# Optimization experiments

Measured on AMD Instinct MI355X. Metric: run time of the kernel, lower is better.

Reference implementation:

```python
import jax, jax.numpy as jnp
import numpy as np

H = 48  # hidden_size


def _lstm_cell(inp, h, c, Wih, Whh, bih, bhh):
    # PyTorch LSTMCell: gates ordered (i, f, g, o)
    gates = inp @ Wih.T + h @ Whh.T + bih + bhh
    i, f, g, o = jnp.split(gates, 4, axis=-1)
    i = jax.nn.sigmoid(i)
    f = jax.nn.sigmoid(f)
    g = jnp.tanh(g)
    o = jax.nn.sigmoid(o)
    c_new = f * c + i * g
    h_new = o * jnp.tanh(c_new)
    return h_new, c_new


def setup_inputs() -> dict:
    key = jax.random.key(0)
    ks = jax.random.split(key, 8)
    B, T = 4096, 512
    s = 0.1
    return {
        "x": jax.random.normal(ks[0], (B, T), dtype=jnp.float32),
        "W_ih0": jax.random.normal(ks[1], (4 * H, 1), dtype=jnp.float32) * s,
        "W_hh0": jax.random.normal(ks[2], (4 * H, H), dtype=jnp.float32) * s,
        "b_ih0": jnp.full((4 * H,), 0.01, dtype=jnp.float32),
        "b_hh0": jnp.full((4 * H,), 0.01, dtype=jnp.float32),
        "W_ih1": jax.random.normal(ks[3], (4 * H, H), dtype=jnp.float32) * s,
        "W_hh1": jax.random.normal(ks[4], (4 * H, H), dtype=jnp.float32) * s,
        "b_ih1": jnp.full((4 * H,), 0.01, dtype=jnp.float32),
        "b_hh1": jnp.full((4 * H,), 0.01, dtype=jnp.float32),
        "W_lin": jax.random.normal(ks[5], (1, H), dtype=jnp.float32) * s,
        "b_lin": jnp.full((1,), 0.01, dtype=jnp.float32),
        "future_pred": 64,
    }


def reference(x, W_ih0, W_hh0, b_ih0, b_hh0, W_ih1, W_hh1, b_ih1, b_hh1,
              W_lin, b_lin, future_pred):
    B = x.shape[0]
    h0 = jnp.zeros((B, H), dtype=jnp.float32)
    c0 = jnp.zeros((B, H), dtype=jnp.float32)
    h1 = jnp.zeros((B, H), dtype=jnp.float32)
    c1 = jnp.zeros((B, H), dtype=jnp.float32)

    def tick(h0, c0, h1, c1, inp):  # inp: [B,1]
        h0, c0 = _lstm_cell(inp, h0, c0, W_ih0, W_hh0, b_ih0, b_hh0)
        h1, c1 = _lstm_cell(h0, h1, c1, W_ih1, W_hh1, b_ih1, b_hh1)
        out = h1 @ W_lin.T + b_lin  # [B,1]
        return h0, c0, h1, c1, out

    # teacher-forced pass over observed sequence
    def step_obs(carry, xt):
        h0, c0, h1, c1 = carry
        h0, c0, h1, c1, out = tick(h0, c0, h1, c1, xt)
        return (h0, c0, h1, c1), out

    xs = jnp.swapaxes(x, 0, 1)[:, :, None]  # [T, B, 1]
    (h0, c0, h1, c1), outs_obs = jax.lax.scan(step_obs, (h0, c0, h1, c1), xs)
    last_out = outs_obs[-1]

    def step_fut(carry, _):
        h0, c0, h1, c1, out = carry
        h0, c0, h1, c1, out = tick(h0, c0, h1, c1, out)
        return (h0, c0, h1, c1, out), out

    _, outs_fut = jax.lax.scan(step_fut, (h0, c0, h1, c1, last_out), None,
                               length=future_pred)

    outs = jnp.concatenate([outs_obs, outs_fut], axis=0)  # [T+F, B, 1]
    return jnp.swapaxes(outs[:, :, 0], 0, 1)  # [B, T+F]
```

## Files before the change

kernel.cpp:

```cpp
#include <hip/hip_runtime.h>

#define T_OBS 512
#define RSTRH 264
#define PSTR  28
#define L2E   1.44269504089f

typedef float    f32x4 __attribute__((ext_vector_type(4)));
typedef _Float16 f16x8 __attribute__((ext_vector_type(8)));

#define MF(A,B,C) __builtin_amdgcn_mfma_f32_16x16x32_f16(A,B,C,0,0,0)

__device__ __forceinline__ unsigned f2h(float f){
    union { _Float16 h; unsigned short u; } v; v.h=(_Float16)f; return (unsigned)v.u;
}

__device__ __forceinline__ float act1(const f32x4 a, float& c){
    const float Ei=__builtin_amdgcn_exp2f(a[0]), Ef=__builtin_amdgcn_exp2f(a[1]);
    const float Eg=__builtin_amdgcn_exp2f(a[2]), Eo=__builtin_amdgcn_exp2f(a[3]);
    const float ui=1.f+Ei, uf=1.f+Ef, ug=1.f+Eg, uo=1.f+Eo;
    const float P=ui*uf, Q=ug*uo;
    const float R=__builtin_amdgcn_rcpf(P*Q);
    const float aP=R*Q, aQ=R*P;
    const float ig=aP*uf, fg=aP*ui;
    const float og=aQ*ug;
    const float gg=fmaf(aQ*uo,-2.f,1.f);
    c = fg*c + ig*gg;
    const float Ec=__builtin_amdgcn_exp2f(2.f*L2E*c);
    return og*fmaf(__builtin_amdgcn_rcpf(1.f+Ec),-2.f,1.f);
}

__device__ __forceinline__ int u_of_pos(const int p){
    return 8*(p>>3) + 4*(p&1) + ((p&7)>>1);
}

__global__ __launch_bounds__(768, 1) void lstm2_v8(
    const float* __restrict__ x,
    const float* __restrict__ Wih0, const float* __restrict__ Whh0,
    const float* __restrict__ bih0, const float* __restrict__ bhh0,
    const float* __restrict__ Wih1, const float* __restrict__ Whh1,
    const float* __restrict__ bih1, const float* __restrict__ bhh1,
    const float* __restrict__ Wlin, const float* __restrict__ blin,
    const int* __restrict__ fut,
    float* __restrict__ out)
{
    __shared__ __attribute__((aligned(16))) _Float16 s_h[16 * RSTRH];
    __shared__ __attribute__((aligned(16))) float s_pr[2][16 * PSTR];
    unsigned* const s32 = (unsigned*)s_h;

    const int tid  = threadIdx.x;
    const int wave = tid >> 6, lane = tid & 63;
    const int q    = lane & 15, rg = lane >> 4;
    const bool isL1 = (wave >= 6);
    const int  w    = isL1 ? wave - 6 : wave;

    for (int i = tid; i < 16 * RSTRH; i += 768) s_h[i] = (_Float16)0.f;

    const float sgl = ((q & 3) == 2) ? 2.f * L2E : -L2E;

    f16x8 ah[2][3], al[2][3];
    #pragma unroll
    for (int i = 0; i < 2; ++i) {
        const int t  = 2 * w + i;
        const int rp = 16 * t + q;
        const int r0 = (rp & 3) * 48 + (rp >> 2);
        #pragma unroll
        for (int s = 0; s < 3; ++s)
            #pragma unroll
            for (int j = 0; j < 8; ++j) {
                const int p = 32 * s + 8 * rg + j;
                float v = 0.f;
                if (isL1) v = ((p < 48) ? Wih1[r0 * 48 + u_of_pos(p)]
                                        : Whh1[r0 * 48 + u_of_pos(p - 48)]) * sgl;
                else if (p < 48) v = Whh0[r0 * 48 + u_of_pos(p)] * sgl;
                const _Float16 hi = (_Float16)v;
                ah[i][s][j] = hi;
                al[i][s][j] = (_Float16)(v - (float)hi);
            }
    }

    const float sg4[4] = { -L2E, -L2E, 2.f * L2E, -L2E };
    f32x4 bvt[2], wi0v[2];
    float wlq[2];
    #pragma unroll
    for (int i = 0; i < 2; ++i) {
        const int u = 8 * w + 4 * i + rg;
        wlq[i] = Wlin[u];
        #pragma unroll
        for (int g = 0; g < 4; ++g) {
            bvt[i][g]  = (isL1 ? (bih1[g*48+u] + bhh1[g*48+u])
                               : (bih0[g*48+u] + bhh0[g*48+u])) * sg4[g];
            wi0v[i][g] = Wih0[g * 48 + u] * sg4[g];
        }
    }

    int koff[3];
    #pragma unroll
    for (int s = 0; s < 3; ++s) {
        const int p0 = 32 * s + 8 * rg;
        koff[s] = p0 + ((p0 >= 48) ? 80 : 0);
    }

    const int F    = fut[0];
    const int TT   = T_OBS + F;
    const int bb0  = blockIdx.x * 16;
    const float bl = blin[0];
    const int xrow = (bb0 + q) * T_OBS;
    const int nbh  = q * RSTRH;
    const int hwp  = nbh + (isL1 ? 128 : 0) + 8 * w + 2 * rg;
    const int prw  = q * PSTR + 4 * w + rg;

    float cc0 = 0.f, cc1 = 0.f;
    const f32x4 z4 = { 0.f, 0.f, 0.f, 0.f };

    __syncthreads();

    if (!isL1) {
        const float x0 = x[xrow];
        const f32x4 a0 = bvt[0] + wi0v[0] * x0;
        const f32x4 a1 = bvt[1] + wi0v[1] * x0;
        const unsigned h0 = f2h(act1(a0, cc0));
        const unsigned h1 = f2h(act1(a1, cc1));
        s32[hwp >> 1] = h0 | (h1 << 16);
    }
    __syncthreads();
    float xcur = isL1 ? 0.f : x[xrow + 1];

#define STEADY(TAU_, CB_, PB_) do {                                              \
    if (!isL1) {                                                                 \
        const float xnxt = x[xrow + (((TAU_) + 1 < T_OBS) ? (TAU_) + 1 : T_OBS - 1)]; \
        if ((TAU_) >= 2 && wave == 0) {           \
            const int nn = lane >> 2, j0 = lane & 3;                             \
            const float* pr = &s_pr[((TAU_) - 1) & 1][nn * PSTR];                \
            float sg = pr[j0] + pr[j0+4] + pr[j0+8] + pr[j0+12]                  \
                     + pr[j0+16] + pr[j0+20];                                    \
            sg += __shfl_xor(sg, 1); sg += __shfl_xor(sg, 2);                    \
            if (j0 == 0) out[(bb0 + nn) * TT + ((TAU_) - 2)] = sg + bl;          \
        }                                                                        \
        const f16x8 B0 = *(const f16x8*)(s_h + nbh + (PB_) + koff[0]);           \
        const f16x8 B1 = *(const f16x8*)(s_h + nbh + (PB_) + koff[1]);           \
        f32x4 Aq[2], Bq[2];                                                      \
        _Pragma("unroll")                                                        \
        for (int i = 0; i < 2; ++i) {                                            \
            Aq[i] = MF(ah[i][0], B0, bvt[i]);                                    \
            Aq[i] = MF(al[i][0], B0, Aq[i]);                                     \
            Bq[i] = MF(ah[i][1], B1, z4);                                        \
            Bq[i] = MF(al[i][1], B1, Bq[i]);                                     \
        }                                                                        \
        const f32x4 a0 = Aq[0] + Bq[0] + wi0v[0] * xcur;                         \
        const f32x4 a1 = Aq[1] + Bq[1] + wi0v[1] * xcur;                         \
        const unsigned h0 = f2h(act1(a0, cc0));                                  \
        const unsigned h1 = f2h(act1(a1, cc1));                                  \
        s32[(hwp + (CB_)) >> 1] = h0 | (h1 << 16);                               \
        xcur = xnxt;                                                             \
    } else {                                                                     \
        const f16x8 B0 = *(const f16x8*)(s_h + nbh + (PB_) + koff[0]);           \
        const f16x8 B1 = *(const f16x8*)(s_h + nbh + (PB_) + koff[1]);           \
        const f16x8 B2 = *(const f16x8*)(s_h + nbh + (PB_) + koff[2]);           \
        f32x4 Aq[2], Bq[2];                                                      \
        _Pragma("unroll")                                                        \
        for (int i = 0; i < 2; ++i) {                                            \
            Aq[i] = MF(ah[i][0], B0, bvt[i]);                                    \
            Aq[i] = MF(al[i][0], B0, Aq[i]);                                     \
            Aq[i] = MF(ah[i][1], B1, Aq[i]);                                     \
            Bq[i] = MF(al[i][1], B1, z4);                                        \
            Bq[i] = MF(ah[i][2], B2, Bq[i]);                                     \
            Bq[i] = MF(al[i][2], B2, Bq[i]);                                     \
        }                                                                        \
        const f32x4 a0 = Aq[0] + Bq[0];                                          \
        const f32x4 a1 = Aq[1] + Bq[1];                                          \
        const float h0 = act1(a0, cc0);                                          \
        const float h1 = act1(a1, cc1);                                          \
        s32[(hwp + (CB_)) >> 1] = f2h(h0) | (f2h(h1) << 16);                     \
        s_pr[(TAU_) & 1][prw] = fmaf(h1, wlq[1], h0 * wlq[0]);                   \
    }                                                                            \
    __syncthreads();                                                             \
} while (0)

    for (int tau = 1; tau < T_OBS - 1; tau += 2) {
        STEADY(tau,     64, 0);
        STEADY(tau + 1,  0, 64);
    }
    STEADY(T_OBS - 1, 64, 0);

    if (tid < 16) {
        const float* pr = &s_pr[1][tid * PSTR];
        const f32x4 sv = *(const f32x4*)(pr)      + *(const f32x4*)(pr + 4)
                       + *(const f32x4*)(pr + 8)  + *(const f32x4*)(pr + 12)
                       + *(const f32x4*)(pr + 16) + *(const f32x4*)(pr + 20);
        out[(bb0 + tid) * TT + (T_OBS - 2)] = sv[0] + sv[1] + sv[2] + sv[3] + bl;
    }

    for (int tau = T_OBS; tau <= TT; ++tau) {
        const int cb = (tau & 1) * 64;
        const int pb = cb ^ 64;

        f32x4 Aq[2], Bq[2];
        if (isL1) {
            const f16x8 B0 = *(const f16x8*)(s_h + nbh + pb + koff[0]);
            const f16x8 B1 = *(const f16x8*)(s_h + nbh + pb + koff[1]);
            const f16x8 B2 = *(const f16x8*)(s_h + nbh + pb + koff[2]);
            #pragma unroll
            for (int i = 0; i < 2; ++i) {
                Aq[i] = MF(ah[i][0], B0, bvt[i]);
                Aq[i] = MF(al[i][0], B0, Aq[i]);
                Aq[i] = MF(ah[i][1], B1, Aq[i]);
                Bq[i] = MF(al[i][1], B1, z4);
                Bq[i] = MF(ah[i][2], B2, Bq[i]);
                Bq[i] = MF(al[i][2], B2, Bq[i]);
            }
            const f32x4 a0 = Aq[0] + Bq[0];
            const f32x4 a1 = Aq[1] + Bq[1];
            const float h0 = act1(a0, cc0);
            const float h1 = act1(a1, cc1);
            s32[(hwp + cb) >> 1] = f2h(h0) | (f2h(h1) << 16);
            s_pr[tau & 1][prw] = fmaf(h1, wlq[1], h0 * wlq[0]);
        } else {
            const f16x8 B0 = *(const f16x8*)(s_h + nbh + pb + koff[0]);
            const f16x8 B1 = *(const f16x8*)(s_h + nbh + pb + koff[1]);
            #pragma unroll
            for (int i = 0; i < 2; ++i) {
                Aq[i] = MF(ah[i][0], B0, bvt[i]);
                Aq[i] = MF(al[i][0], B0, Aq[i]);
                Bq[i] = MF(ah[i][1], B1, z4);
                Bq[i] = MF(al[i][1], B1, Bq[i]);
            }
        }
        __syncthreads();

        if (!isL1) {
            const float* pr = &s_pr[tau & 1][q * PSTR];
            const f32x4 sv = *(const f32x4*)(pr)      + *(const f32x4*)(pr + 4)
                           + *(const f32x4*)(pr + 8)  + *(const f32x4*)(pr + 12)
                           + *(const f32x4*)(pr + 16) + *(const f32x4*)(pr + 20);
            const float o = sv[0] + sv[1] + sv[2] + sv[3] + bl;
            if (tid < 16) out[(bb0 + q) * TT + (tau - 1)] = o;
            if (tau < TT) {
                const f32x4 a0 = Aq[0] + Bq[0] + wi0v[0] * o;
                const f32x4 a1 = Aq[1] + Bq[1] + wi0v[1] * o;
                const unsigned h0 = f2h(act1(a0, cc0));
                const unsigned h1 = f2h(act1(a1, cc1));
                s32[(hwp + cb) >> 1] = h0 | (h1 << 16);
            }
        }
        __syncthreads();
    }
}

extern "C" void kernel_launch(void* const* d_in, const int* in_sizes, int n_in,
                              void* d_out, int out_size, void* d_ws, size_t ws_size,
                              hipStream_t stream) {
    const float* x    = (const float*)d_in[0];
    const float* Wih0 = (const float*)d_in[1];
    const float* Whh0 = (const float*)d_in[2];
    const float* bih0 = (const float*)d_in[3];
    const float* bhh0 = (const float*)d_in[4];
    const float* Wih1 = (const float*)d_in[5];
    const float* Whh1 = (const float*)d_in[6];
    const float* bih1 = (const float*)d_in[7];
    const float* bhh1 = (const float*)d_in[8];
    const float* Wlin = (const float*)d_in[9];
    const float* blin = (const float*)d_in[10];
    const int*   fut  = (const int*)d_in[11];
    float* out = (float*)d_out;

    const int B    = in_sizes[0] / T_OBS;
    const int grid = B / 16;
    lstm2_v8<<<grid, 768, 0, stream>>>(
        x, Wih0, Whh0, bih0, bhh0, Wih1, Whh1, bih1, bhh1, Wlin, blin, fut, out);
}
```

Before: 512.9 us.

## Replace block barriers with LDS counter spin-waits and triple-buffered hidden state

```diff
diff --git a/kernel.cpp b/kernel.cpp
--- a/kernel.cpp
+++ b/kernel.cpp
@@ -1,7 +1,7 @@
 #include <hip/hip_runtime.h>
 
 #define T_OBS 512
-#define RSTRH 264
+#define RSTRH 296
 #define PSTR  28
 #define L2E   1.44269504089f
 
@@ -33,7 +33,16 @@
     return 8*(p>>3) + 4*(p&1) + ((p&7)>>1);
 }
 
-__global__ __launch_bounds__(768, 1) void lstm2_v8(
+__device__ __forceinline__ void spin_ge(volatile unsigned* pc, unsigned t0, unsigned t1){
+    unsigned v = *pc;
+    while (((v & 0xffffu) < t0) || ((v >> 16) < t1)) {
+        __builtin_amdgcn_s_sleep(1);
+        v = *pc;
+    }
+    asm volatile("" ::: "memory");
+}
+
+__global__ __launch_bounds__(768, 1) void lstm2_v9(
     const float* __restrict__ x,
     const float* __restrict__ Wih0, const float* __restrict__ Whh0,
     const float* __restrict__ bih0, const float* __restrict__ bhh0,
@@ -44,8 +53,10 @@
     float* __restrict__ out)
 {
     __shared__ __attribute__((aligned(16))) _Float16 s_h[16 * RSTRH];
-    __shared__ __attribute__((aligned(16))) float s_pr[2][16 * PSTR];
+    __shared__ __attribute__((aligned(16))) float s_pr[3][16 * PSTR];
+    __shared__ unsigned s_cnt;
     unsigned* const s32 = (unsigned*)s_h;
+    volatile unsigned* const pcv = (volatile unsigned*)&s_cnt;
 
     const int tid  = threadIdx.x;
     const int wave = tid >> 6, lane = tid & 63;
@@ -54,6 +65,7 @@
     const int  w    = isL1 ? wave - 6 : wave;
 
     for (int i = tid; i < 16 * RSTRH; i += 768) s_h[i] = (_Float16)0.f;
+    if (tid == 0) s_cnt = 0u;
 
     const float sgl = ((q & 3) == 2) ? 2.f * L2E : -L2E;
 
@@ -93,24 +105,17 @@
         }
     }
 
-    int koff[3];
-    #pragma unroll
-    for (int s = 0; s < 3; ++s) {
-        const int p0 = 32 * s + 8 * rg;
-        koff[s] = p0 + ((p0 >= 48) ? 80 : 0);
-    }
-
+    const int ko0 = 8 * rg, ko1 = 32 + 8 * rg, ko2 = 64 + 8 * rg;
     const int F    = fut[0];
     const int TT   = T_OBS + F;
     const int bb0  = blockIdx.x * 16;
     const float bl = blin[0];
     const int xrow = (bb0 + q) * T_OBS;
     const int nbh  = q * RSTRH;
-    const int hwp  = nbh + (isL1 ? 128 : 0) + 8 * w + 2 * rg;
+    const int hw0  = nbh + 8 * w + 2 * rg;
     const int prw  = q * PSTR + 4 * w + rg;
 
     float cc0 = 0.f, cc1 = 0.f;
-    const f32x4 z4 = { 0.f, 0.f, 0.f, 0.f };
 
     __syncthreads();
 
@@ -118,131 +123,146 @@
         const float x0 = x[xrow];
         const f32x4 a0 = bvt[0] + wi0v[0] * x0;
         const f32x4 a1 = bvt[1] + wi0v[1] * x0;
-        const unsigned h0 = f2h(act1(a0, cc0));
-        const unsigned h1 = f2h(act1(a1, cc1));
-        s32[hwp >> 1] = h0 | (h1 << 16);
-    }
-    __syncthreads();
+        const unsigned h0p = f2h(act1(a0, cc0));
+        const unsigned h1p = f2h(act1(a1, cc1));
+        s32[hw0 >> 1] = h0p | (h1p << 16);
+        asm volatile("s_waitcnt lgkmcnt(0)" ::: "memory");
+        if (lane == 0) atomicAdd(&s_cnt, 1u);
+    } else {
+        if (lane == 0) atomicAdd(&s_cnt, 1u << 16);
+    }
     float xcur = isL1 ? 0.f : x[xrow + 1];
 
-#define STEADY(TAU_, CB_, PB_) do {                                              \
+#define STEADY(TAU_, WR_, RR_, GB_) do {                                         \
+    const unsigned t0_ = 6u * (unsigned)(TAU_);                                  \
     if (!isL1) {                                                                 \
+        spin_ge(pcv, t0_, t0_ - 6u);                                             \
         const float xnxt = x[xrow + (((TAU_) + 1 < T_OBS) ? (TAU_) + 1 : T_OBS - 1)]; \
-        if ((TAU_) >= 2 && wave == 0) {           \
-            const int nn = lane >> 2, j0 = lane & 3;                             \
-            const float* pr = &s_pr[((TAU_) - 1) & 1][nn * PSTR];                \
-            float sg = pr[j0] + pr[j0+4] + pr[j0+8] + pr[j0+12]                  \
-                     + pr[j0+16] + pr[j0+20];                                    \
-            sg += __shfl_xor(sg, 1); sg += __shfl_xor(sg, 2);                    \
-            if (j0 == 0) out[(bb0 + nn) * TT + ((TAU_) - 2)] = sg + bl;          \
+        const f16x8 B0 = *(const f16x8*)(s_h + nbh + 96*(RR_) + ko0);            \
+        const f16x8 B1 = *(const f16x8*)(s_h + nbh + 96*(RR_) + ko1);            \
+        f32x4 g0 = MF(ah[0][0], B0, bvt[0]);                                     \
+        g0 = MF(al[0][0], B0, g0);                                               \
+        g0 = MF(ah[0][1], B1, g0);                                               \
+        g0 = MF(al[0][1], B1, g0);                                               \
+        f32x4 g1 = MF(ah[1][0], B0, bvt[1]);                                     \
+        g1 = MF(al[1][0], B0, g1);                                               \
+        g1 = MF(ah[1][1], B1, g1);                                               \
+        g1 = MF(al[1][1], B1, g1);                                               \
+        if ((TAU_) >= 3 && w < 4) {                \
+            const int nn = 4 * w + rg;                                           \
+            const float* pr = &s_pr[GB_][nn * PSTR];                             \
+            float gv = pr[q] + ((q < 8) ? pr[16 + q] : 0.f);                     \
+            gv += __shfl_xor(gv, 1); gv += __shfl_xor(gv, 2);                    \
+            gv += __shfl_xor(gv, 4); gv += __shfl_xor(gv, 8);                    \
+            if (q == 0) out[(bb0 + nn) * TT + ((TAU_) - 3)] = gv + bl;           \
         }                                                                        \
-        const f16x8 B0 = *(const f16x8*)(s_h + nbh + (PB_) + koff[0]);           \
-        const f16x8 B1 = *(const f16x8*)(s_h + nbh + (PB_) + koff[1]);           \
-        f32x4 Aq[2], Bq[2];                                                      \
-        _Pragma("unroll")                                                        \
-        for (int i = 0; i < 2; ++i) {                                            \
-            Aq[i] = MF(ah[i][0], B0, bvt[i]);                                    \
-            Aq[i] = MF(al[i][0], B0, Aq[i]);                                     \
-            Bq[i] = MF(ah[i][1], B1, z4);                                        \
-            Bq[i] = MF(al[i][1], B1, Bq[i]);                                     \
-        }                                                                        \
-        const f32x4 a0 = Aq[0] + Bq[0] + wi0v[0] * xcur;                         \
-        const f32x4 a1 = Aq[1] + Bq[1] + wi0v[1] * xcur;                         \
-        const unsigned h0 = f2h(act1(a0, cc0));                                  \
-        const unsigned h1 = f2h(act1(a1, cc1));                                  \
-        s32[(hwp + (CB_)) >> 1] = h0 | (h1 << 16);                               \
+        g0 += wi0v[0] * xcur;                                                    \
+        g1 += wi0v[1] * xcur;                                                    \
+        const unsigned h0p = f2h(act1(g0, cc0));                                 \
+        const unsigned h1p = f2h(act1(g1, cc1));                                 \
+        s32[(hw0 + 96*(WR_)) >> 1] = h0p | (h1p << 16);                          \
+        asm volatile("s_waitcnt lgkmcnt(0)" ::: "memory");                       \
+        if (lane == 0) atomicAdd(&s_cnt, 1u);                                    \
         xcur = xnxt;                                                             \
     } else {                                                                     \
-        const f16x8 B0 = *(const f16x8*)(s_h + nbh + (PB_) + koff[0]);           \
-        const f16x8 B1 = *(const f16x8*)(s_h + nbh + (PB_) + koff[1]);           \
-        const f16x8 B2 = *(const f16x8*)(s_h + nbh + (PB_) + koff[2]);           \
-        f32x4 Aq[2], Bq[2];                                                      \
-        _Pragma("unroll")                                                        \
-        for (int i = 0; i < 2; ++i) {                                            \
-            Aq[i] = MF(ah[i][0], B0, bvt[i]);                                    \
-            Aq[i] = MF(al[i][0], B0, Aq[i]);                                     \
-            Aq[i] = MF(ah[i][1], B1, Aq[i]);                                     \
-            Bq[i] = MF(al[i][1], B1, z4);                                        \
-            Bq[i] = MF(ah[i][2], B2, Bq[i]);                                     \
-            Bq[i] = MF(al[i][2], B2, Bq[i]);                                     \
-        }                                                                        \
-        const f32x4 a0 = Aq[0] + Bq[0];                                          \
-        const f32x4 a1 = Aq[1] + Bq[1];                                          \
-        const float h0 = act1(a0, cc0);                                          \
-        const float h1 = act1(a1, cc1);                                          \
-        s32[(hwp + (CB_)) >> 1] = f2h(h0) | (f2h(h1) << 16);                     \
-        s_pr[(TAU_) & 1][prw] = fmaf(h1, wlq[1], h0 * wlq[0]);                   \
+        spin_ge(pcv, t0_, t0_);                                                  \
+        const f16x8 B0 = *(const f16x8*)(s_h + nbh + 96*(RR_) + ko0);            \
+        const f16x8 B1 = *(const f16x8*)(s_h + nbh + 96*(RR_) + ko1);            \
+        const f16x8 B2 = *(const f16x8*)(s_h + nbh + 96*(RR_) + ko2);            \
+        f32x4 g0 = MF(ah[0][0], B0, bvt[0]);                                     \
+        g0 = MF(al[0][0], B0, g0);                                               \
+        g0 = MF(ah[0][1], B1, g0);                                               \
+        g0 = MF(al[0][1], B1, g0);                                               \
+        g0 = MF(ah[0][2], B2, g0);                                               \
+        g0 = MF(al[0][2], B2, g0);                                               \
+        f32x4 g1 = MF(ah[1][0], B0, bvt[1]);                                     \
+        g1 = MF(al[1][0], B0, g1);                                               \
+        g1 = MF(ah[1][1], B1, g1);                                               \
+        g1 = MF(al[1][1], B1, g1);                                               \
+        g1 = MF(ah[1][2], B2, g1);                                               \
+        g1 = MF(al[1][2], B2, g1);                                               \
+        const float h0f = act1(g0, cc0);                                         \
+        const float h1f = act1(g1, cc1);                                         \
+        s32[(hw0 + 96*(WR_) + 48) >> 1] = f2h(h0f) | (f2h(h1f) << 16);           \
+        s_pr[WR_][prw] = fmaf(h1f, wlq[1], h0f * wlq[0]);                        \
+        asm volatile("s_waitcnt lgkmcnt(0)" ::: "memory");                       \
+        if (lane == 0) atomicAdd(&s_cnt, 1u << 16);                              \
     }                                                                            \
-    __syncthreads();                                                             \
 } while (0)
 
-    for (int tau = 1; tau < T_OBS - 1; tau += 2) {
-        STEADY(tau,     64, 0);
-        STEADY(tau + 1,  0, 64);
-    }
-    STEADY(T_OBS - 1, 64, 0);
-
-    if (tid < 16) {
-        const float* pr = &s_pr[1][tid * PSTR];
-        const f32x4 sv = *(const f32x4*)(pr)      + *(const f32x4*)(pr + 4)
-                       + *(const f32x4*)(pr + 8)  + *(const f32x4*)(pr + 12)
-                       + *(const f32x4*)(pr + 16) + *(const f32x4*)(pr + 20);
-        out[(bb0 + tid) * TT + (T_OBS - 2)] = sv[0] + sv[1] + sv[2] + sv[3] + bl;
-    }
-
+    for (int tau = 1; tau + 2 <= T_OBS - 1; tau += 3) {
+        STEADY(tau,     1, 0, 2);
+        STEADY(tau + 1, 2, 1, 0);
+        STEADY(tau + 2, 0, 2, 1);
+    }
+    STEADY(T_OBS - 1, 1, 0, 2);
+
+    int wr = 2, rr = 1;
     for (int tau = T_OBS; tau <= TT; ++tau) {
-        const int cb = (tau & 1) * 64;
-        const int pb = cb ^ 64;
-
-        f32x4 Aq[2], Bq[2];
+        const unsigned t0_ = 6u * (unsigned)tau;
         if (isL1) {
-            const f16x8 B0 = *(const f16x8*)(s_h + nbh + pb + koff[0]);
-            const f16x8 B1 = *(const f16x8*)(s_h + nbh + pb + koff[1]);
-            const f16x8 B2 = *(const f16x8*)(s_h + nbh + pb + koff[2]);
-            #pragma unroll
-            for (int i = 0; i < 2; ++i) {
-                Aq[i] = MF(ah[i][0], B0, bvt[i]);
-                Aq[i] = MF(al[i][0], B0, Aq[i]);
-                Aq[i] = MF(ah[i][1], B1, Aq[i]);
-                Bq[i] = MF(al[i][1], B1, z4);
-                Bq[i] = MF(ah[i][2], B2, Bq[i]);
-                Bq[i] = MF(al[i][2], B2, Bq[i]);
+            spin_ge(pcv, t0_, t0_);
+            const f16x8 B0 = *(const f16x8*)(s_h + nbh + 96*rr + ko0);
+            const f16x8 B1 = *(const f16x8*)(s_h + nbh + 96*rr + ko1);
+            const f16x8 B2 = *(const f16x8*)(s_h + nbh + 96*rr + ko2);
+            f32x4 g0 = MF(ah[0][0], B0, bvt[0]);
+            g0 = MF(al[0][0], B0, g0);
+            g0 = MF(ah[0][1], B1, g0);
+            g0 = MF(al[0][1], B1, g0);
+            g0 = MF(ah[0][2], B2, g0);
+            g0 = MF(al[0][2], B2, g0);
+            f32x4 g1 = MF(ah[1][0], B0, bvt[1]);
+            g1 = MF(al[1][0], B0, g1);
+            g1 = MF(ah[1][1], B1, g1);
+            g1 = MF(al[1][1], B1, g1);
+            g1 = MF(ah[1][2], B2, g1);
+            g1 = MF(al[1][2], B2, g1);
+            const float h0f = act1(g0, cc0);
+            const float h1f = act1(g1, cc1);
+            s32[(hw0 + 96*wr + 48) >> 1] = f2h(h0f) | (f2h(h1f) << 16);
+            s_pr[wr][prw] = fmaf(h1f, wlq[1], h0f * wlq[0]);
+            asm volatile("s_waitcnt lgkmcnt(0)" ::: "memory");
+            if (lane == 0) atomicAdd(&s_cnt, 1u << 16);
+        } else {
+            spin_ge(pcv, t0_, t0_ - 6u);
+            const f16x8 B0 = *(const f16x8*)(s_h + nbh + 96*rr + ko0);
+            const f16x8 B1 = *(const f16x8*)(s_h + nbh + 96*rr + ko1);
+            f32x4 g0 = MF(ah[0][0], B0, bvt[0]);
+            g0 = MF(al[0][0], B0, g0);
+            g0 = MF(ah[0][1], B1, g0);
+            g0 = MF(al[0][1], B1, g0);
+            f32x4 g1 = MF(ah[1][0], B0, bvt[1]);
+            g1 = MF(al[1][0], B0, g1);
+            g1 = MF(ah[1][1], B1, g1);
+            g1 = MF(al[1][1], B1, g1);
+            if ((tau == T_OBS || tau == T_OBS + 1) && w < 4) {
+                const int gb = (tau - 2) % 3;
+                const int nn = 4 * w + rg;
+                const float* pr = &s_pr[gb][nn * PSTR];
+                float gv = pr[q] + ((q < 8) ? pr[16 + q] : 0.f);
+                gv += __shfl_xor(gv, 1); gv += __shfl_xor(gv, 2);
+                gv += __shfl_xor(gv, 4); gv += __shfl_xor(gv, 8);
+                if (q == 0) out[(bb0 + nn) * TT + (tau - 3)] = gv + bl;
             }
-            const f32x4 a0 = Aq[0] + Bq[0];
-            const f32x4 a1 = Aq[1] + Bq[1];
-            const float h0 = act1(a0, cc0);
-            const float h1 = act1(a1, cc1);
-            s32[(hwp + cb) >> 1] = f2h(h0) | (f2h(h1) << 16);
-            s_pr[tau & 1][prw] = fmaf(h1, wlq[1], h0 * wlq[0]);
-        } else {
-            const f16x8 B0 = *(const f16x8*)(s_h + nbh + pb + koff[0]);
-            const f16x8 B1 = *(const f16x8*)(s_h + nbh + pb + koff[1]);
-            #pragma unroll
-            for (int i = 0; i < 2; ++i) {
-                Aq[i] = MF(ah[i][0], B0, bvt[i]);
-                Aq[i] = MF(al[i][0], B0, Aq[i]);
-                Bq[i] = MF(ah[i][1], B1, z4);
-                Bq[i] = MF(al[i][1], B1, Bq[i]);
-            }
-        }
-        __syncthreads();
-
-        if (!isL1) {
-            const float* pr = &s_pr[tau & 1][q * PSTR];
+            spin_ge(pcv, t0_, t0_ + 6u);
+            const float* pr = &s_pr[wr][q * PSTR];
             const f32x4 sv = *(const f32x4*)(pr)      + *(const f32x4*)(pr + 4)
                            + *(const f32x4*)(pr + 8)  + *(const f32x4*)(pr + 12)
                            + *(const f32x4*)(pr + 16) + *(const f32x4*)(pr + 20);
             const float o = sv[0] + sv[1] + sv[2] + sv[3] + bl;
             if (tid < 16) out[(bb0 + q) * TT + (tau - 1)] = o;
             if (tau < TT) {
-                const f32x4 a0 = Aq[0] + Bq[0] + wi0v[0] * o;
-                const f32x4 a1 = Aq[1] + Bq[1] + wi0v[1] * o;
-                const unsigned h0 = f2h(act1(a0, cc0));
-                const unsigned h1 = f2h(act1(a1, cc1));
-                s32[(hwp + cb) >> 1] = h0 | (h1 << 16);
+                g0 += wi0v[0] * o;
+                g1 += wi0v[1] * o;
+                const unsigned h0p = f2h(act1(g0, cc0));
+                const unsigned h1p = f2h(act1(g1, cc1));
+                s32[(hw0 + 96*wr) >> 1] = h0p | (h1p << 16);
             }
+            asm volatile("s_waitcnt lgkmcnt(0)" ::: "memory");
+            if (lane == 0) atomicAdd(&s_cnt, 1u);
         }
-        __syncthreads();
+        wr = (wr == 2) ? 0 : wr + 1;
+        rr = (rr == 2) ? 0 : rr + 1;
     }
 }
 
@@ -265,6 +285,6 @@
 
     const int B    = in_sizes[0] / T_OBS;
     const int grid = B / 16;
-    lstm2_v8<<<grid, 768, 0, stream>>>(
+    lstm2_v9<<<grid, 768, 0, stream>>>(
         x, Wih0, Whh0, bih0, bhh0, Wih1, Whh1, bih1, bhh1, Wlin, blin, fut, out);
 }
```

New measurement: 592.3 us. 15.5% more time.
